# Kernel optimization log

Measured on AMD Instinct MI355X. Metric: run time of the kernel, lower is better.

## Reference

```python
import jax, jax.numpy as jnp
import numpy as np

IN_CH, OUT_CH = 64, 64
MODES1, MODES2 = 20, 20
B, H, W = 16, 256, 256


def setup_inputs() -> dict:
    key = jax.random.key(0)
    k_x, k1r, k1i, k2r, k2i = jax.random.split(key, 5)
    scale = 1.0 / (IN_CH * OUT_CH)
    wshape = (IN_CH, OUT_CH, MODES1, MODES2)
    return {
        "x": jax.random.normal(k_x, (B, IN_CH, H, W), dtype=jnp.float32),
        "w1r": scale * jax.random.uniform(k1r, wshape, dtype=jnp.float32),
        "w1i": scale * jax.random.uniform(k1i, wshape, dtype=jnp.float32),
        "w2r": scale * jax.random.uniform(k2r, wshape, dtype=jnp.float32),
        "w2i": scale * jax.random.uniform(k2i, wshape, dtype=jnp.float32),
    }


def reference(x, w1r, w1i, w2r, w2i):
    # x: [B, C_in, H, W] real
    b, _, size1, size2 = x.shape
    m1, m2 = w1r.shape[2], w1r.shape[3]
    out_ch = w1r.shape[1]

    x_ft = jnp.fft.rfft2(x)  # [B, C_in, H, W//2+1] complex
    w1 = (w1r + 1j * w1i).astype(jnp.complex64)
    w2 = (w2r + 1j * w2i).astype(jnp.complex64)

    # Complex spectral mixing on the retained low-frequency corners
    top = jnp.einsum("bixy,ioxy->boxy", x_ft[:, :, :m1, :m2], w1)
    bot = jnp.einsum("bixy,ioxy->boxy", x_ft[:, :, -m1:, :m2], w2)

    out_ft = jnp.zeros((b, out_ch, size1, size2 // 2 + 1), dtype=jnp.complex64)
    out_ft = out_ft.at[:, :, :m1, :m2].set(top)
    out_ft = out_ft.at[:, :, -m1:, :m2].set(bot)

    return jnp.fft.irfft2(out_ft, s=(size1, size2))  # [B, C_out, H, W]
```

## Files before the change

### kernel.cpp

```cpp
#include <hip/hip_runtime.h>
#include <cstddef>


constexpr float KTH = 6.28318530717958647692f / 256.0f;

__global__ __launch_bounds__(320) void dft_w_kernel(const float* __restrict__ x,
                                                    float2* __restrict__ X1) {
  __shared__ float uds[128 * 68];
  __shared__ float xs0[128];
  const int tid = threadIdx.x;
  const int sl = tid / 10;
  const int kp = tid - sl * 10;
  const size_t row0 = (size_t)blockIdx.x * 128;
  const float* xb = x + row0 * 256;

  float cr0, sr0, cr1, sr1;
  __sincosf((float)(2 * kp) * KTH, &sr0, &cr0);
  __sincosf((float)(2 * kp + 1) * KTH, &sr1, &cr1);

  float re[4][2] = {};
  float im[4][2] = {};

  const int swc = sl & 3;
  const float* ub = uds + sl * 4 * 68;

  for (int c = 0; c < 4; ++c) {
    __syncthreads();
    if (tid < 256) {
      const int row = tid >> 1;
      const int hf = tid & 1;
      const int base = c * 32 + hf * 16;
      const float* xr = xb + (size_t)row * 256;
      float4 fq0 = *(const float4*)(xr + base);
      float4 fq1 = *(const float4*)(xr + base + 4);
      float4 fq2 = *(const float4*)(xr + base + 8);
      float4 fq3 = *(const float4*)(xr + base + 12);
      float4 fq4 = *(const float4*)(xr + base + 16);
      const float* xm = xr + (240 - base);
      float4 mq0 = *(const float4*)(xm);
      float4 mq1 = *(const float4*)(xm + 4);
      float4 mq2 = *(const float4*)(xm + 8);
      float4 mq3 = *(const float4*)(xm + 12);
      if (c == 0 && hf == 0) xs0[row] = fq0.x;
      float* urow = uds + row * 68;
      const int sw = (row >> 2) & 3;
#define STAGE_Q(q, fa, fb, m)                                         \
      {                                                               \
        float4 u, d;                                                  \
        u.x = fa.y + m.w; d.x = fa.y - m.w;                           \
        u.y = fa.z + m.z; d.y = fa.z - m.z;                           \
        u.z = fa.w + m.y; d.z = fa.w - m.y;                           \
        u.w = fb.x + m.x; d.w = fb.x - m.x;                           \
        if (c == 3 && hf == 1 && (q) == 3) u.w *= 0.5f;    \
        int col = (((hf * 4 + (q)) ^ sw) * 4);                        \
        *(float4*)(urow + col) = u;                                   \
        *(float4*)(urow + 32 + col) = d;                              \
      }
      STAGE_Q(0, fq0, fq1, mq3)
      STAGE_Q(1, fq1, fq2, mq2)
      STAGE_Q(2, fq2, fq3, mq1)
      STAGE_Q(3, fq3, fq4, mq0)
#undef STAGE_Q
    }
    __syncthreads();

    for (int g = 0; g < 2; ++g) {
      const int w1 = c * 32 + g * 16 + 1;
      float c0, s0, c1, s1;
      { int m = (2 * kp * w1) & 255;       __sincosf((float)m * KTH, &s0, &c0); }
      { int m = ((2 * kp + 1) * w1) & 255; __sincosf((float)m * KTH, &s1, &c1); }
#pragma unroll
      for (int q = 0; q < 4; ++q) {
        const int col = (((g * 4 + q) ^ swc) * 4);
        float4 u0 = *(const float4*)(ub + col);
        float4 d0 = *(const float4*)(ub + 32 + col);
        float4 u1 = *(const float4*)(ub + 68 + col);
        float4 d1 = *(const float4*)(ub + 68 + 32 + col);
        float4 u2 = *(const float4*)(ub + 136 + col);
        float4 d2 = *(const float4*)(ub + 136 + 32 + col);
        float4 u3 = *(const float4*)(ub + 204 + col);
        float4 d3 = *(const float4*)(ub + 204 + 32 + col);
#define DSTEP(e)                                                      \
        {                                                             \
          re[0][0] = fmaf(u0.e, c0, re[0][0]);                        \
          im[0][0] = fmaf(d0.e, s0, im[0][0]);                        \
          re[1][0] = fmaf(u1.e, c0, re[1][0]);                        \
          im[1][0] = fmaf(d1.e, s0, im[1][0]);                        \
          re[2][0] = fmaf(u2.e, c0, re[2][0]);                        \
          im[2][0] = fmaf(d2.e, s0, im[2][0]);                        \
          re[3][0] = fmaf(u3.e, c0, re[3][0]);                        \
          im[3][0] = fmaf(d3.e, s0, im[3][0]);                        \
          re[0][1] = fmaf(u0.e, c1, re[0][1]);                        \
          im[0][1] = fmaf(d0.e, s1, im[0][1]);                        \
          re[1][1] = fmaf(u1.e, c1, re[1][1]);                        \
          im[1][1] = fmaf(d1.e, s1, im[1][1]);                        \
          re[2][1] = fmaf(u2.e, c1, re[2][1]);                        \
          im[2][1] = fmaf(d2.e, s1, im[2][1]);                        \
          re[3][1] = fmaf(u3.e, c1, re[3][1]);                        \
          im[3][1] = fmaf(d3.e, s1, im[3][1]);                        \
          float cn0 = c0 * cr0 - s0 * sr0;                            \
          s0 = fmaf(c0, sr0, s0 * cr0);                               \
          c0 = cn0;                                                   \
          float cn1 = c1 * cr1 - s1 * sr1;                            \
          s1 = fmaf(c1, sr1, s1 * cr1);                               \
          c1 = cn1;                                                   \
        }
        DSTEP(x) DSTEP(y) DSTEP(z) DSTEP(w)
#undef DSTEP
      }
    }
  }

#pragma unroll
  for (int r = 0; r < 4; ++r) {
    float x0v = xs0[sl * 4 + r];
    size_t ob = (row0 + (size_t)(sl * 4 + r)) * 20 + (size_t)(kp * 2);
    float4 o;
    o.x = re[r][0] + x0v;
    o.y = -im[r][0];
    o.z = re[r][1] + x0v;
    o.w = -im[r][1];
    *(float4*)(X1 + ob) = o;
  }
}

__global__ __launch_bounds__(448) void dft_h_kernel(const float2* __restrict__ X1,
                                                    float2* __restrict__ X2) {
  __shared__ float4 Xs4[256 * 10];
  int bc = blockIdx.x;
  const float4* src = (const float4*)(X1 + (size_t)bc * 5120);
  for (int i = threadIdx.x; i < 2560; i += 448) Xs4[i] = src[i];
  __syncthreads();

  int t = threadIdx.x;
  if (t < 400) {
    int ky_i = t / 10;
    int g    = t % 10;
    int ky = (ky_i < 20) ? ky_i : 216 + ky_i;
    float cr, srn;
    __sincosf((float)ky * KTH, &srn, &cr);
    srn = -srn;
    float ar0 = 0.f, ai0 = 0.f, ar1 = 0.f, ai1 = 0.f;
    for (int h0 = 0; h0 < 256; h0 += 16) {
      int m = (ky * h0) & 255;
      float c, s;
      __sincosf((float)m * KTH, &s, &c);
      s = -s;
#pragma unroll
      for (int dh = 0; dh < 16; ++dh) {
        float4 v = Xs4[(h0 + dh) * 10 + g];
        ar0 = fmaf(v.x, c, fmaf(-v.y, s, ar0));
        ai0 = fmaf(v.x, s, fmaf(v.y, c, ai0));
        ar1 = fmaf(v.z, c, fmaf(-v.w, s, ar1));
        ai1 = fmaf(v.z, s, fmaf(v.w, c, ai1));
        float cn = c * cr - s * srn;
        s = fmaf(c, srn, s * cr);
        c = cn;
      }
    }
    size_t ob = (size_t)bc * 800 + (size_t)ky_i * 20 + (size_t)g * 2;
    X2[ob]     = make_float2(ar0, ai0);
    X2[ob + 1] = make_float2(ar1, ai1);
  }
}

__global__ __launch_bounds__(256) void mix_kernel(const float2* __restrict__ X2,
                                                  const float* __restrict__ w1r,
                                                  const float* __restrict__ w1i,
                                                  const float* __restrict__ w2r,
                                                  const float* __restrict__ w2i,
                                                  float2* __restrict__ Z) {
  __shared__ float2 Xs[16 * 64];
  __shared__ float Wr[64 * 64];
  __shared__ float Wi[64 * 64];
  int blk = blockIdx.x;
  int j = blk / 20, kx = blk % 20;
  const float* wr; const float* wi; int moff;
  if (j < 20) { wr = w1r; wi = w1i; moff = j * 20 + kx; }
  else        { wr = w2r; wi = w2i; moff = (j - 20) * 20 + kx; }

  for (int io = threadIdx.x; io < 4096; io += 256) {
    Wr[io] = wr[(size_t)io * 400 + moff];
    Wi[io] = wi[(size_t)io * 400 + moff];
  }
  for (int bi = threadIdx.x; bi < 1024; bi += 256) {
    Xs[bi] = X2[(size_t)bi * 800 + blk];
  }
  __syncthreads();

  int b  = threadIdx.x >> 4;
  int o0 = (threadIdx.x & 15) * 4;
  float zr[4] = {0, 0, 0, 0}, zi[4] = {0, 0, 0, 0};
  for (int i = 0; i < 64; ++i) {
    float2 xv = Xs[b * 64 + i];
#pragma unroll
    for (int q = 0; q < 4; ++q) {
      float wrv = Wr[i * 64 + o0 + q];
      float wiv = Wi[i * 64 + o0 + q];
      zr[q] = fmaf(xv.x, wrv, fmaf(-xv.y, wiv, zr[q]));
      zi[q] = fmaf(xv.x, wiv, fmaf(xv.y, wrv, zi[q]));
    }
  }
#pragma unroll
  for (int q = 0; q < 4; ++q) {
    Z[(size_t)(b * 64 + o0 + q) * 800 + blk] = make_float2(zr[q], zi[q]);
  }
}

__global__ __launch_bounds__(256) void icd_kernel(const float2* __restrict__ Z,
                                                  float* __restrict__ out) {
  __shared__ float2 Zs[800];
  __shared__ float4 Ys4[256 * 11];
  int bo = blockIdx.x;
  const float2* src = Z + (size_t)bo * 800;
  for (int i = threadIdx.x; i < 800; i += 256) Zs[i] = src[i];
  __syncthreads();

  const float SC = 2.0f / 65536.0f;
  float* outb = out + (size_t)bo * 65536;

  {
    int h = threadIdx.x;
    float cr, sr;
    __sincosf((float)h * KTH, &sr, &cr);
    float accr[20], acci[20];
#pragma unroll
    for (int k = 0; k < 20; ++k) { accr[k] = 0.f; acci[k] = 0.f; }
    float c = 1.0f, s = 0.0f;
    for (int j = 0; j < 40; ++j) {
      if (j == 20) {
        int m = (236 * h) & 255;
        __sincosf((float)m * KTH, &s, &c);
      }
#pragma unroll
      for (int k = 0; k < 20; ++k) {
        float2 z = Zs[j * 20 + k];
        accr[k] = fmaf(z.x, c, fmaf(-z.y, s, accr[k]));
        acci[k] = fmaf(z.x, s, fmaf(z.y, c, acci[k]));
      }
      float cn = c * cr - s * sr;
      s = fmaf(c, sr, s * cr);
      c = cn;
    }
    float2* yrow = (float2*)(Ys4 + h * 11);
    yrow[0] = make_float2(0.5f * accr[0], 0.5f * acci[0]);
#pragma unroll
    for (int k = 1; k < 20; ++k) yrow[k] = make_float2(accr[k], acci[k]);
    float sum0 = 0.5f * accr[0];
    float sum128 = 0.5f * accr[0];
#pragma unroll
    for (int k = 1; k < 20; ++k) {
      sum0 += accr[k];
      sum128 += (k & 1) ? -accr[k] : accr[k];
    }
    outb[h * 256] = sum0 * SC;
    outb[h * 256 + 128] = sum128 * SC;
  }
  __syncthreads();

  {
    int t = threadIdx.x;
    int hg = t >> 7;
    int wt = t & 127;
    if (wt != 0) {
      float cw, sw;
      __sincosf((float)wt * KTH, &sw, &cw);
      float c2 = cw * cw - sw * sw;
      float s2 = 2.0f * cw * sw;
      int h0e = hg * 128;
      for (int h0 = h0e; h0 < h0e + 128; h0 += 8) {
        float P[8], Q[8];
#pragma unroll
        for (int r = 0; r < 8; ++r) { P[r] = 0.f; Q[r] = 0.f; }
        float c0 = 1.0f, s0 = 0.0f;
        float c1 = cw,   s1 = sw;
        const float4* yb = Ys4 + h0 * 11;
        for (int p = 0; p < 10; ++p) {
#pragma unroll
          for (int r = 0; r < 8; ++r) {
            float4 y = yb[r * 11 + p];
            P[r] = fmaf(y.x, c0, P[r]);
            Q[r] = fmaf(y.y, s0, Q[r]);
            P[r] = fmaf(y.z, c1, P[r]);
            Q[r] = fmaf(y.w, s1, Q[r]);
          }
          float cn0 = c0 * c2 - s0 * s2;
          s0 = fmaf(c0, s2, s0 * c2);
          c0 = cn0;
          float cn1 = c1 * c2 - s1 * s2;
          s1 = fmaf(c1, s2, s1 * c2);
          c1 = cn1;
        }
#pragma unroll
        for (int r = 0; r < 8; ++r) {
          float pv = P[r] * SC, qv = Q[r] * SC;
          outb[(h0 + r) * 256 + wt] = pv - qv;
          outb[(h0 + r) * 256 + 256 - wt] = pv + qv;
        }
      }
    }
  }
}

extern "C" void kernel_launch(void* const* d_in, const int* in_sizes, int n_in,
                              void* d_out, int out_size, void* d_ws, size_t ws_size,
                              hipStream_t stream) {
  const float* x   = (const float*)d_in[0];
  const float* w1r = (const float*)d_in[1];
  const float* w1i = (const float*)d_in[2];
  const float* w2r = (const float*)d_in[3];
  const float* w2i = (const float*)d_in[4];
  float* out = (float*)d_out;

  float2* X1  = (float2*)d_out;
  float2* wsc = (float2*)d_ws;
  float2* X2  = wsc;
  float2* Zb  = wsc + 819200;

  dft_w_kernel<<<2048, 320, 0, stream>>>(x, X1);
  dft_h_kernel<<<1024, 448, 0, stream>>>(X1, X2);
  mix_kernel  <<<800, 256, 0, stream>>>(X2, w1r, w1i, w2r, w2i, Zb);
  icd_kernel  <<<1024, 256, 0, stream>>>(Zb, out);
}
```

Baseline: 679.9 us.

## Exploit conjugate symmetry in inverse DFT to halve column work and restructure row pass

The column pass of the inverse transform now runs only on h in 0..128. Each thread keeps the four separate real/imag products, so it can write both row h and its mirror 256-h, which halves the column DFT work. The row pass is reorganised so each thread owns one output row and evaluates 64 frequencies, using the even/odd split of k to produce four outputs per evaluation (w, 256-w, 128±w). This removes the strided 8-row shared-memory reads, but it doubles the per-thread register arrays and makes stores row-contiguous per thread, which are uncoalesced across threads.

```diff
diff --git a/kernel.cpp b/kernel.cpp
--- a/kernel.cpp
+++ b/kernel.cpp
@@ -210,7 +210,7 @@
 __global__ __launch_bounds__(256) void icd_kernel(const float2* __restrict__ Z,
                                                   float* __restrict__ out) {
   __shared__ float2 Zs[800];
-  __shared__ float4 Ys4[256 * 11];
+  __shared__ float4 Ys4[256 * 10];
   int bo = blockIdx.x;
   const float2* src = Z + (size_t)bo * 800;
   for (int i = threadIdx.x; i < 800; i += 256) Zs[i] = src[i];
@@ -218,14 +218,15 @@
 
   const float SC = 2.0f / 65536.0f;
   float* outb = out + (size_t)bo * 65536;
-
-  {
-    int h = threadIdx.x;
+  int t = threadIdx.x;
+
+  if (t <= 128) {
+    int h = t;
     float cr, sr;
     __sincosf((float)h * KTH, &sr, &cr);
-    float accr[20], acci[20];
-#pragma unroll
-    for (int k = 0; k < 20; ++k) { accr[k] = 0.f; acci[k] = 0.f; }
+    float A[20], Bv[20], Cc[20], Dd[20];
+#pragma unroll
+    for (int k = 0; k < 20; ++k) { A[k] = 0.f; Bv[k] = 0.f; Cc[k] = 0.f; Dd[k] = 0.f; }
     float c = 1.0f, s = 0.0f;
     for (int j = 0; j < 40; ++j) {
       if (j == 20) {
@@ -235,70 +236,86 @@
 #pragma unroll
       for (int k = 0; k < 20; ++k) {
         float2 z = Zs[j * 20 + k];
-        accr[k] = fmaf(z.x, c, fmaf(-z.y, s, accr[k]));
-        acci[k] = fmaf(z.x, s, fmaf(z.y, c, acci[k]));
+        A[k]  = fmaf(z.x, c, A[k]);
+        Bv[k] = fmaf(z.y, s, Bv[k]);
+        Cc[k] = fmaf(z.y, c, Cc[k]);
+        Dd[k] = fmaf(z.x, s, Dd[k]);
       }
       float cn = c * cr - s * sr;
       s = fmaf(c, sr, s * cr);
       c = cn;
     }
-    float2* yrow = (float2*)(Ys4 + h * 11);
-    yrow[0] = make_float2(0.5f * accr[0], 0.5f * acci[0]);
-#pragma unroll
-    for (int k = 1; k < 20; ++k) yrow[k] = make_float2(accr[k], acci[k]);
-    float sum0 = 0.5f * accr[0];
-    float sum128 = 0.5f * accr[0];
+    {
+      float4* y1 = Ys4 + h * 10;
+#pragma unroll
+      for (int p = 0; p < 10; ++p) {
+        float r0 = A[2 * p] - Bv[2 * p], i0 = Cc[2 * p] + Dd[2 * p];
+        float r1 = A[2 * p + 1] - Bv[2 * p + 1], i1 = Cc[2 * p + 1] + Dd[2 * p + 1];
+        if (p == 0) { r0 *= 0.5f; i0 *= 0.5f; }
+        y1[p] = make_float4(r0, i0, r1, i1);
+      }
+    }
+    if (t >= 1 && t < 128) {
+      float4* y2 = Ys4 + (256 - h) * 10;
+#pragma unroll
+      for (int p = 0; p < 10; ++p) {
+        float r0 = A[2 * p] + Bv[2 * p], i0 = Cc[2 * p] - Dd[2 * p];
+        float r1 = A[2 * p + 1] + Bv[2 * p + 1], i1 = Cc[2 * p + 1] - Dd[2 * p + 1];
+        if (p == 0) { r0 *= 0.5f; i0 *= 0.5f; }
+        y2[p] = make_float4(r0, i0, r1, i1);
+      }
+    }
+  }
+  __syncthreads();
+
+  float Yr[20], Yi[20];
+  {
+    const float4* yb = Ys4 + t * 10;
+#pragma unroll
+    for (int p = 0; p < 10; ++p) {
+      float4 y = yb[p];
+      Yr[2 * p] = y.x; Yi[2 * p] = y.y;
+      Yr[2 * p + 1] = y.z; Yi[2 * p + 1] = y.w;
+    }
+  }
+  float* orow = outb + (size_t)t * 256;
+  {
+    float s0 = Yr[0], s128 = Yr[0];
 #pragma unroll
     for (int k = 1; k < 20; ++k) {
-      sum0 += accr[k];
-      sum128 += (k & 1) ? -accr[k] : accr[k];
-    }
-    outb[h * 256] = sum0 * SC;
-    outb[h * 256 + 128] = sum128 * SC;
-  }
-  __syncthreads();
-
-  {
-    int t = threadIdx.x;
-    int hg = t >> 7;
-    int wt = t & 127;
-    if (wt != 0) {
-      float cw, sw;
-      __sincosf((float)wt * KTH, &sw, &cw);
-      float c2 = cw * cw - sw * sw;
-      float s2 = 2.0f * cw * sw;
-      int h0e = hg * 128;
-      for (int h0 = h0e; h0 < h0e + 128; h0 += 8) {
-        float P[8], Q[8];
-#pragma unroll
-        for (int r = 0; r < 8; ++r) { P[r] = 0.f; Q[r] = 0.f; }
-        float c0 = 1.0f, s0 = 0.0f;
-        float c1 = cw,   s1 = sw;
-        const float4* yb = Ys4 + h0 * 11;
-        for (int p = 0; p < 10; ++p) {
-#pragma unroll
-          for (int r = 0; r < 8; ++r) {
-            float4 y = yb[r * 11 + p];
-            P[r] = fmaf(y.x, c0, P[r]);
-            Q[r] = fmaf(y.y, s0, Q[r]);
-            P[r] = fmaf(y.z, c1, P[r]);
-            Q[r] = fmaf(y.w, s1, Q[r]);
-          }
-          float cn0 = c0 * c2 - s0 * s2;
-          s0 = fmaf(c0, s2, s0 * c2);
-          c0 = cn0;
-          float cn1 = c1 * c2 - s1 * s2;
-          s1 = fmaf(c1, s2, s1 * c2);
-          c1 = cn1;
-        }
-#pragma unroll
-        for (int r = 0; r < 8; ++r) {
-          float pv = P[r] * SC, qv = Q[r] * SC;
-          outb[(h0 + r) * 256 + wt] = pv - qv;
-          outb[(h0 + r) * 256 + 256 - wt] = pv + qv;
-        }
-      }
-    }
+      s0 += Yr[k];
+      s128 += (k & 1) ? -Yr[k] : Yr[k];
+    }
+    orow[0] = s0 * SC;
+    orow[128] = s128 * SC;
+  }
+  float c1, s1;
+  __sincosf(KTH, &s1, &c1);
+  float cw = c1, sw = s1;
+  for (int w = 1; w <= 64; ++w) {
+    if (w > 1 && (w & 15) == 1) __sincosf((float)w * KTH, &sw, &cw);
+    float Pe = Yr[0], Po = 0.f, Qe = 0.f, Qo = 0.f;
+    float c = cw, s = sw;
+#pragma unroll
+    for (int k = 1; k < 20; ++k) {
+      if (k == 10) {
+        int m = (10 * w) & 255;
+        __sincosf((float)m * KTH, &s, &c);
+      }
+      if (k & 1) { Po = fmaf(Yr[k], c, Po); Qo = fmaf(Yi[k], s, Qo); }
+      else       { Pe = fmaf(Yr[k], c, Pe); Qe = fmaf(Yi[k], s, Qe); }
+      float cn = c * cw - s * sw;
+      s = fmaf(c, sw, s * cw);
+      c = cn;
+    }
+    float sm = Pe + Po, dm = Pe - Po, sq = Qe + Qo, dq = Qe - Qo;
+    orow[w]       = (sm - sq) * SC;
+    orow[256 - w] = (sm + sq) * SC;
+    orow[128 + w] = (dm - dq) * SC;
+    orow[128 - w] = (dm + dq) * SC;
+    float cn = cw * c1 - sw * s1;
+    sw = fmaf(cw, s1, sw * c1);
+    cw = cn;
   }
 }
 
```

Measured after the change: 1.617 ms. +137.9%, slower.
